# Performance work log

Measured on AMD Instinct MI355X. Metric: run time of the kernel, lower is better.

## Reference

```python
import jax, jax.numpy as jnp
import numpy as np

N, S, E, H = 4, 2048, 1024, 16
D = E // H  # head dim = 64


def setup_inputs() -> dict:
    key = jax.random.key(0)
    ks = jax.random.split(key, 8)
    return {
        "values": jax.random.normal(ks[0], (N, S, E), dtype=jnp.float32),
        "keys": jax.random.normal(ks[1], (N, S, E), dtype=jnp.float32),
        "queries": jax.random.normal(ks[2], (N, S, E), dtype=jnp.float32),
        "mask": jnp.ones((N, 1, 1, S), dtype=jnp.int32),
        "Wv": jax.random.normal(ks[3], (D, D), dtype=jnp.float32) / np.sqrt(D),
        "Wk": jax.random.normal(ks[4], (D, D), dtype=jnp.float32) / np.sqrt(D),
        "Wq": jax.random.normal(ks[5], (D, D), dtype=jnp.float32) / np.sqrt(D),
        "W_out": jax.random.normal(ks[6], (E, E), dtype=jnp.float32) / np.sqrt(E),
        "b_out": jnp.zeros((E,), dtype=jnp.float32),
    }


def reference(values, keys, queries, mask, Wv, Wk, Wq, W_out, b_out):
    n, q_len = queries.shape[0], queries.shape[1]
    v = values.reshape(n, -1, H, D)
    k = keys.reshape(n, -1, H, D)
    q = queries.reshape(n, q_len, H, D)
    # per-head linear projections (torch Linear: x @ W.T), shared across heads
    v = jnp.einsum('nlhd,ed->nlhe', v, Wv)
    k = jnp.einsum('nlhd,ed->nlhe', k, Wk)
    q = jnp.einsum('nqhd,ed->nqhe', q, Wq)
    # full score tensor [n, h, q, k], faithful to the original einsum
    energy = jnp.einsum('nqhd,nkhd->nhqk', q, k)
    energy = jnp.where(mask == 0, jnp.float32(-1e20), energy)
    # NOTE: original scales by sqrt(embed_size), not sqrt(head_dim)
    attention = jax.nn.softmax(energy / jnp.sqrt(jnp.float32(E)), axis=3)
    out = jnp.einsum('nhql,nlhd->nqhd', attention, v).reshape(n, q_len, E)
    out = out @ W_out.T + b_out
    return out
```

## Files before the change

### kernel.cpp

```cpp
#include <hip/hip_runtime.h>
#include <stdint.h>

#define N_B 4
#define SEQ 2048
#define EMB 1024
#define NH  16
#define HD  64
#define NHT 64
#define BQ  128
#define BK  64

typedef __attribute__((ext_vector_type(8))) short bf16x8;
typedef __attribute__((ext_vector_type(4))) short bf16x4;
typedef __attribute__((ext_vector_type(4))) float f32x4;

__device__ __forceinline__ short f2bf(float x) {
  unsigned u = __float_as_uint(x);
  u += 0x7fffu + ((u >> 16) & 1u);
  return (short)(u >> 16);
}

#if __has_builtin(__builtin_amdgcn_cvt_pk_bf16_f32)
typedef __attribute__((ext_vector_type(2))) __bf16 bf16v2;
__device__ __forceinline__ unsigned pkbf(float a, float b) {
  bf16v2 r = __builtin_amdgcn_cvt_pk_bf16_f32(a, b);
  union { bf16v2 v; unsigned u; } c; c.v = r; return c.u;
}
#else
__device__ __forceinline__ unsigned pkbf(float a, float b) {
  return (unsigned)(unsigned short)f2bf(a) | ((unsigned)(unsigned short)f2bf(b) << 16);
}
#endif

__device__ __forceinline__ void glds16(const short* g, short* l) {
  __builtin_amdgcn_global_load_lds(
      (const __attribute__((address_space(1))) unsigned int*)g,
      (__attribute__((address_space(3))) unsigned int*)l, 16, 0, 0);
}

__device__ __forceinline__ int swz_src(int lane) {
  return (((lane & 7) ^ ((lane >> 3) & 7)) * 8) + ((lane >> 3) * 64);
}
__device__ __forceinline__ int swz_rd(int r, int k) {
  return r * 64 + ((k ^ (r & 7)) * 8);
}

__global__ __launch_bounds__(256) void projm_kernel(
    const float* __restrict__ Xq, const float* __restrict__ Xk, const float* __restrict__ Xv,
    const float* __restrict__ Wq, const float* __restrict__ Wk, const float* __restrict__ Wv,
    short* __restrict__ Qp, short* __restrict__ Kp, short* __restrict__ Vp,
    const float* __restrict__ Wo, short* __restrict__ Wb) {
  int tid = threadIdx.x;
  int z = blockIdx.z;
  if (z == 3) {
    int flat = blockIdx.x + blockIdx.y * 16;
    int idx = (flat * 256 + tid) * 4;
    f32x4 v = *(const f32x4*)(Wo + idx);
    uint2 u; u.x = pkbf(v.x, v.y); u.y = pkbf(v.z, v.w);
    *(uint2*)(Wb + idx) = u;
    return;
  }
  const float* X = (z == 0) ? Xq : (z == 1) ? Xk : Xv;
  const float* W = (z == 0) ? Wq : (z == 1) ? Wk : Wv;
  short* out = (z == 0) ? Qp : (z == 1) ? Kp : Vp;
  int transposed = (z == 2);

  __shared__ __attribute__((aligned(16))) short Xs[128 * 64];
  __shared__ __attribute__((aligned(16))) short Ws[64 * 64];
  int w = tid >> 6, lane = tid & 63;
  int quad = lane >> 4, l15 = lane & 15;
  int sb = blockIdx.x * 128;
  int nh = blockIdx.y;
  int n = nh >> 4, h = nh & 15;
  int r4 = tid >> 2, c0 = (tid & 3) * 16;
  int ch0 = c0 >> 3;
#pragma unroll
  for (int rr = 0; rr < 2; rr++) {
    int row = rr * 64 + r4;
    const float* gp = X + ((size_t)(n * SEQ + sb + row)) * EMB + h * HD + c0;
    f32x4 a = *(const f32x4*)gp, b = *(const f32x4*)(gp + 4);
    f32x4 c = *(const f32x4*)(gp + 8), d = *(const f32x4*)(gp + 12);
    uint4 u0, u1;
    u0.x = pkbf(a.x, a.y); u0.y = pkbf(a.z, a.w);
    u0.z = pkbf(b.x, b.y); u0.w = pkbf(b.z, b.w);
    u1.x = pkbf(c.x, c.y); u1.y = pkbf(c.z, c.w);
    u1.z = pkbf(d.x, d.y); u1.w = pkbf(d.z, d.w);
    *(uint4*)&Xs[row * 64 + ((ch0 ^ (row & 7)) * 8)] = u0;
    *(uint4*)&Xs[row * 64 + (((ch0 + 1) ^ (row & 7)) * 8)] = u1;
  }
  {
    int e = r4;
    const float* wp = W + e * HD + c0;
    f32x4 a = *(const f32x4*)wp, b = *(const f32x4*)(wp + 4);
    f32x4 c = *(const f32x4*)(wp + 8), d = *(const f32x4*)(wp + 12);
    uint4 u0, u1;
    u0.x = pkbf(a.x, a.y); u0.y = pkbf(a.z, a.w);
    u0.z = pkbf(b.x, b.y); u0.w = pkbf(b.z, b.w);
    u1.x = pkbf(c.x, c.y); u1.y = pkbf(c.z, c.w);
    u1.z = pkbf(d.x, d.y); u1.w = pkbf(d.z, d.w);
    *(uint4*)&Ws[e * 64 + ((ch0 ^ (e & 7)) * 8)] = u0;
    *(uint4*)&Ws[e * 64 + (((ch0 + 1) ^ (e & 7)) * 8)] = u1;
  }
  __syncthreads();
  f32x4 acc[2][4] = {};
#pragma unroll
  for (int ch = 0; ch < 2; ch++) {
    bf16x8 af[2], bfr[4];
#pragma unroll
    for (int mi = 0; mi < 2; mi++)
      af[mi] = *(const bf16x8*)&Xs[swz_rd(w * 32 + mi * 16 + l15, ch * 4 + quad)];
#pragma unroll
    for (int ni = 0; ni < 4; ni++)
      bfr[ni] = *(const bf16x8*)&Ws[swz_rd(ni * 16 + l15, ch * 4 + quad)];
#pragma unroll
    for (int mi = 0; mi < 2; mi++)
#pragma unroll
      for (int ni = 0; ni < 4; ni++)
        acc[mi][ni] = __builtin_amdgcn_mfma_f32_16x16x32_bf16(af[mi], bfr[ni], acc[mi][ni], 0, 0, 0);
  }
  if (!transposed) {
#pragma unroll
    for (int mi = 0; mi < 2; mi++)
#pragma unroll
      for (int ni = 0; ni < 4; ni++)
#pragma unroll
        for (int r = 0; r < 4; r++) {
          int s = sb + w * 32 + mi * 16 + quad * 4 + r;
          out[((size_t)nh * SEQ + s) * HD + ni * 16 + l15] = f2bf(acc[mi][ni][r]);
        }
  } else {
#pragma unroll
    for (int mi = 0; mi < 2; mi++)
#pragma unroll
      for (int ni = 0; ni < 4; ni++) {
        int e2 = ni * 16 + l15;
        int s0 = sb + w * 32 + mi * 16 + quad * 4;
        uint2 u;
        u.x = pkbf(acc[mi][ni][0], acc[mi][ni][1]);
        u.y = pkbf(acc[mi][ni][2], acc[mi][ni][3]);
        *(uint2*)(out + ((size_t)nh * HD + e2) * SEQ + s0) = u;
      }
  }
}

__global__ __launch_bounds__(256, 4) void attn_kernel(
    const short* __restrict__ Qg, const short* __restrict__ Kg,
    const short* __restrict__ Vg, const int* __restrict__ maskp,
    short* __restrict__ AO) {
  __shared__ __attribute__((aligned(16))) short Ks[64 * 64];
  __shared__ __attribute__((aligned(16))) short Vts[64 * 64];
  __shared__ __attribute__((aligned(16))) short QP[128 * 64];

  int tid = threadIdx.x;
  int w = tid >> 6, lane = tid & 63;
  int quad = lane >> 4, l15 = lane & 15;
  int nh = blockIdx.x;
  int qt0 = blockIdx.y * BQ;
  int n = nh >> 4, h = nh & 15;
  const float csc = 0.04508422f;
  int ssrc = swz_src(lane);
  int vrow = lane >> 3;
  int vcg = (((lane & 7) ^ ((lane >> 3) & 7)) * 8);
  const int NT = SEQ / BK;

  const short* kb = Kg + (size_t)nh * SEQ * HD;
  const short* vb = Vg + (size_t)nh * HD * SEQ;

  const short* qbase = Qg + ((size_t)nh * SEQ + qt0) * HD;
#pragma unroll
  for (int i = 0; i < 4; i++) {
    int idx = (w * 4 + i) * 512;
    glds16(qbase + idx + ssrc, &QP[idx]);
  }
  int mcur = maskp[n * SEQ + lane];
  __syncthreads();
  bf16x8 qf[2][2];
#pragma unroll
  for (int nt = 0; nt < 2; nt++)
#pragma unroll
    for (int ch = 0; ch < 2; ch++)
      qf[nt][ch] = *(const bf16x8*)&QP[swz_rd(w * 32 + nt * 16 + l15, ch * 4 + quad)];

  bf16x8 vone;
#pragma unroll
  for (int j = 0; j < 8; j++) vone[j] = (short)0x3F80;

  f32x4 Oacc[2][4] = {};
  f32x4 lacc[2] = {};
  short* psw = &QP[w * 2048];

  for (int kt = 0; kt < NT; kt++) {
    int k0 = kt * BK;
    __syncthreads();
#pragma unroll
    for (int i = 0; i < 2; i++) {
      int idx = (w * 2 + i) * 512;
      glds16(kb + (size_t)k0 * HD + idx + ssrc, &Ks[idx]);
      int d = (w * 2 + i) * 8 + vrow;
      glds16(vb + (size_t)d * SEQ + k0 + vcg, &Vts[idx]);
    }
    int knx = (kt + 1 < NT) ? kt + 1 : kt;
    int mnxt = maskp[n * SEQ + knx * BK + lane];
    __syncthreads();

    unsigned long long mb = __ballot(mcur != 0);

    f32x4 st[4][2];
#pragma unroll
    for (int mt = 0; mt < 4; mt++) {
      bf16x8 kf0 = *(const bf16x8*)&Ks[swz_rd(mt * 16 + l15, quad)];
      bf16x8 kf1 = *(const bf16x8*)&Ks[swz_rd(mt * 16 + l15, 4 + quad)];
#pragma unroll
      for (int nt = 0; nt < 2; nt++) {
        f32x4 a = {0.f, 0.f, 0.f, 0.f};
        a = __builtin_amdgcn_mfma_f32_16x16x32_bf16(kf0, qf[nt][0], a, 0, 0, 0);
        a = __builtin_amdgcn_mfma_f32_16x16x32_bf16(kf1, qf[nt][1], a, 0, 0, 0);
        st[mt][nt] = a;
      }
    }
    if (mb != ~0ull) {
#pragma unroll
      for (int mt = 0; mt < 4; mt++)
#pragma unroll
        for (int r = 0; r < 4; r++) {
          int kk = mt * 16 + quad * 4 + r;
          if (!((mb >> kk) & 1)) { st[mt][0][r] = -1e20f; st[mt][1][r] = -1e20f; }
        }
    }
#pragma unroll
    for (int nt = 0; nt < 2; nt++) {
      int wrow = nt * 16 + l15;
#pragma unroll
      for (int mt = 0; mt < 4; mt++) {
        float p0 = __builtin_amdgcn_exp2f(st[mt][nt][0] * csc);
        float p1 = __builtin_amdgcn_exp2f(st[mt][nt][1] * csc);
        float p2 = __builtin_amdgcn_exp2f(st[mt][nt][2] * csc);
        float p3 = __builtin_amdgcn_exp2f(st[mt][nt][3] * csc);
        uint2 u;
        u.x = pkbf(p0, p1);
        u.y = pkbf(p2, p3);
        *(uint2*)&psw[wrow * 64 + (((mt * 2 + (quad >> 1)) ^ (wrow & 7)) * 8) + (quad & 1) * 4] = u;
      }
    }
    __builtin_amdgcn_wave_barrier();

#pragma unroll
    for (int ch = 0; ch < 2; ch++) {
      bf16x8 pf[2];
#pragma unroll
      for (int qt = 0; qt < 2; qt++)
        pf[qt] = *(const bf16x8*)&psw[swz_rd(qt * 16 + l15, ch * 4 + quad)];
#pragma unroll
      for (int qt = 0; qt < 2; qt++)
        lacc[qt] = __builtin_amdgcn_mfma_f32_16x16x32_bf16(pf[qt], vone, lacc[qt], 0, 0, 0);
#pragma unroll
      for (int dt = 0; dt < 4; dt++) {
        bf16x8 vf = *(const bf16x8*)&Vts[swz_rd(dt * 16 + l15, ch * 4 + quad)];
#pragma unroll
        for (int qt = 0; qt < 2; qt++)
          Oacc[qt][dt] = __builtin_amdgcn_mfma_f32_16x16x32_bf16(pf[qt], vf, Oacc[qt][dt], 0, 0, 0);
      }
    }
    mcur = mnxt;
  }
#pragma unroll
  for (int qt = 0; qt < 2; qt++)
#pragma unroll
    for (int r = 0; r < 4; r++) {
      float inv = 1.0f / lacc[qt][r];
      int qrow = qt0 + w * 32 + qt * 16 + quad * 4 + r;
      size_t rowb = ((size_t)n * SEQ + qrow) * EMB + h * HD;
#pragma unroll
      for (int dt = 0; dt < 4; dt++)
        AO[rowb + dt * 16 + l15] = f2bf(Oacc[qt][dt][r] * inv);
    }
}

__global__ __launch_bounds__(256, 2) void gemm_kernel(const short* __restrict__ A,
                                                      const short* __restrict__ B,
                                                      const float* __restrict__ bias,
                                                      float* __restrict__ C) {
  __shared__ __attribute__((aligned(16))) short As[2][128 * 64];
  __shared__ __attribute__((aligned(16))) short Bs[2][128 * 64];
  int tid = threadIdx.x;
  int w = tid >> 6, lane = tid & 63;
  int quad = lane >> 4, l15 = lane & 15;
  int m0 = blockIdx.x * 128, n0 = blockIdx.y * 128;
  int mw = (w & 1) * 64, nw = (w >> 1) * 64;
  int lrow = lane >> 3;
  int lcg = ((lane & 7) ^ ((lane >> 3) & 7)) * 8;
  f32x4 acc[4][4] = {};
#pragma unroll
  for (int i = 0; i < 4; i++) {
    int ii = w * 4 + i;
    int r = ii * 8 + lrow;
    glds16(A + (size_t)(m0 + r) * 1024 + lcg, &As[0][ii * 512]);
    glds16(B + (size_t)(n0 + r) * 1024 + lcg, &Bs[0][ii * 512]);
  }
  __syncthreads();
  for (int kt = 0; kt < 16; kt++) {
    int cur = kt & 1;
    if (kt < 15) {
      int k0n = (kt + 1) * 64;
#pragma unroll
      for (int i = 0; i < 4; i++) {
        int ii = w * 4 + i;
        int r = ii * 8 + lrow;
        glds16(A + (size_t)(m0 + r) * 1024 + k0n + lcg, &As[cur ^ 1][ii * 512]);
        glds16(B + (size_t)(n0 + r) * 1024 + k0n + lcg, &Bs[cur ^ 1][ii * 512]);
      }
    }
#pragma unroll
    for (int ch = 0; ch < 2; ch++) {
      bf16x8 af[4], bfr[4];
#pragma unroll
      for (int mi = 0; mi < 4; mi++)
        af[mi] = *(const bf16x8*)&As[cur][swz_rd(mw + mi * 16 + l15, ch * 4 + quad)];
#pragma unroll
      for (int ni = 0; ni < 4; ni++)
        bfr[ni] = *(const bf16x8*)&Bs[cur][swz_rd(nw + ni * 16 + l15, ch * 4 + quad)];
#pragma unroll
      for (int mi = 0; mi < 4; mi++)
#pragma unroll
        for (int ni = 0; ni < 4; ni++)
          acc[mi][ni] = __builtin_amdgcn_mfma_f32_16x16x32_bf16(af[mi], bfr[ni], acc[mi][ni], 0, 0, 0);
    }
    __syncthreads();
  }
#pragma unroll
  for (int ni = 0; ni < 4; ni++) {
    int col = n0 + nw + ni * 16 + l15;
    float bv = bias[col];
#pragma unroll
    for (int mi = 0; mi < 4; mi++) {
      int rb = m0 + mw + mi * 16 + quad * 4;
#pragma unroll
      for (int r = 0; r < 4; r++)
        C[(size_t)(rb + r) * 1024 + col] = acc[mi][ni][r] + bv;
    }
  }
}

extern "C" void kernel_launch(void* const* d_in, const int* in_sizes, int n_in,
                              void* d_out, int out_size, void* d_ws, size_t ws_size,
                              hipStream_t stream) {
  const float* values  = (const float*)d_in[0];
  const float* keys    = (const float*)d_in[1];
  const float* queries = (const float*)d_in[2];
  const int*   mask    = (const int*)d_in[3];
  const float* Wv = (const float*)d_in[4];
  const float* Wk = (const float*)d_in[5];
  const float* Wq = (const float*)d_in[6];
  const float* Wo = (const float*)d_in[7];
  const float* bo = (const float*)d_in[8];
  float* out = (float*)d_out;

  short* ws = (short*)d_ws;
  short* Qp = ws;
  short* Kp = Qp + (size_t)NHT * SEQ * HD;
  short* Vp = Kp + (size_t)NHT * SEQ * HD;
  short* AO = Vp + (size_t)NHT * SEQ * HD;
  short* Wb = AO + (size_t)N_B * SEQ * EMB;

  dim3 pg(SEQ / 128, NHT, 4);
  projm_kernel<<<pg, dim3(256), 0, stream>>>(queries, keys, values, Wq, Wk, Wv,
                                             Qp, Kp, Vp, Wo, Wb);
  dim3 ag(NHT, SEQ / BQ);
  attn_kernel<<<ag, dim3(256), 0, stream>>>(Qp, Kp, Vp, mask, AO);
  dim3 gg(8192 / 128, 1024 / 128);
  gemm_kernel<<<gg, dim3(256), 0, stream>>>(AO, Wb, bo, out);
}
```

Baseline: 284.0 us.

## Double-buffer K/V tiles in attention and fold softmax scale into Q

The attention loop now keeps two K/V tile buffers in one shared LDS array. It prefetches the next tile while computing on the current one, so each iteration needs one block barrier instead of two. The P staging buffer is split into two halves per wave, and s_setprio is raised around the MFMA sections. The softmax scale is applied in the Q projection before bf16 rounding, which removes one multiply per score. The cost is more LDS per block, and Q is rounded after scaling, which shifts precision slightly.

```diff
diff --git a/kernel.cpp b/kernel.cpp
--- a/kernel.cpp
+++ b/kernel.cpp
@@ -64,6 +64,7 @@
   const float* W = (z == 0) ? Wq : (z == 1) ? Wk : Wv;
   short* out = (z == 0) ? Qp : (z == 1) ? Kp : Vp;
   int transposed = (z == 2);
+  float oscale = (z == 0) ? 0.04508422f : 1.0f;
 
   __shared__ __attribute__((aligned(16))) short Xs[128 * 64];
   __shared__ __attribute__((aligned(16))) short Ws[64 * 64];
@@ -126,7 +127,7 @@
 #pragma unroll
         for (int r = 0; r < 4; r++) {
           int s = sb + w * 32 + mi * 16 + quad * 4 + r;
-          out[((size_t)nh * SEQ + s) * HD + ni * 16 + l15] = f2bf(acc[mi][ni][r]);
+          out[((size_t)nh * SEQ + s) * HD + ni * 16 + l15] = f2bf(acc[mi][ni][r] * oscale);
         }
   } else {
 #pragma unroll
@@ -147,9 +148,7 @@
     const short* __restrict__ Qg, const short* __restrict__ Kg,
     const short* __restrict__ Vg, const int* __restrict__ maskp,
     short* __restrict__ AO) {
-  __shared__ __attribute__((aligned(16))) short Ks[64 * 64];
-  __shared__ __attribute__((aligned(16))) short Vts[64 * 64];
-  __shared__ __attribute__((aligned(16))) short QP[128 * 64];
+  __shared__ __attribute__((aligned(16))) short L[20480];
 
   int tid = threadIdx.x;
   int w = tid >> 6, lane = tid & 63;
@@ -157,7 +156,6 @@
   int nh = blockIdx.x;
   int qt0 = blockIdx.y * BQ;
   int n = nh >> 4, h = nh & 15;
-  const float csc = 0.04508422f;
   int ssrc = swz_src(lane);
   int vrow = lane >> 3;
   int vcg = (((lane & 7) ^ ((lane >> 3) & 7)) * 8);
@@ -165,12 +163,20 @@
 
   const short* kb = Kg + (size_t)nh * SEQ * HD;
   const short* vb = Vg + (size_t)nh * HD * SEQ;
+  short* Pw = &L[16384 + w * 1024];
 
   const short* qbase = Qg + ((size_t)nh * SEQ + qt0) * HD;
 #pragma unroll
   for (int i = 0; i < 4; i++) {
     int idx = (w * 4 + i) * 512;
-    glds16(qbase + idx + ssrc, &QP[idx]);
+    glds16(qbase + idx + ssrc, &L[8192 + idx]);
+  }
+#pragma unroll
+  for (int i = 0; i < 2; i++) {
+    int idx = (w * 2 + i) * 512;
+    glds16(kb + idx + ssrc, &L[idx]);
+    int d = (w * 2 + i) * 8 + vrow;
+    glds16(vb + (size_t)d * SEQ + vcg, &L[4096 + idx]);
   }
   int mcur = maskp[n * SEQ + lane];
   __syncthreads();
@@ -179,7 +185,8 @@
   for (int nt = 0; nt < 2; nt++)
 #pragma unroll
     for (int ch = 0; ch < 2; ch++)
-      qf[nt][ch] = *(const bf16x8*)&QP[swz_rd(w * 32 + nt * 16 + l15, ch * 4 + quad)];
+      qf[nt][ch] = *(const bf16x8*)&L[8192 + swz_rd(w * 32 + nt * 16 + l15, ch * 4 + quad)];
+  __syncthreads();
 
   bf16x8 vone;
 #pragma unroll
@@ -187,81 +194,95 @@
 
   f32x4 Oacc[2][4] = {};
   f32x4 lacc[2] = {};
-  short* psw = &QP[w * 2048];
 
   for (int kt = 0; kt < NT; kt++) {
-    int k0 = kt * BK;
-    __syncthreads();
-#pragma unroll
-    for (int i = 0; i < 2; i++) {
-      int idx = (w * 2 + i) * 512;
-      glds16(kb + (size_t)k0 * HD + idx + ssrc, &Ks[idx]);
-      int d = (w * 2 + i) * 8 + vrow;
-      glds16(vb + (size_t)d * SEQ + k0 + vcg, &Vts[idx]);
+    int cur = kt & 1;
+    const short* Kb = &L[cur * 8192];
+    const short* Vb = &L[cur * 8192 + 4096];
+    if (kt + 1 < NT) {
+      size_t k0n = (size_t)(kt + 1) * BK;
+      short* Kn = &L[(cur ^ 1) * 8192];
+#pragma unroll
+      for (int i = 0; i < 2; i++) {
+        int idx = (w * 2 + i) * 512;
+        glds16(kb + k0n * HD + idx + ssrc, &Kn[idx]);
+        int d = (w * 2 + i) * 8 + vrow;
+        glds16(vb + (size_t)d * SEQ + k0n + vcg, &Kn[4096 + idx]);
+      }
     }
     int knx = (kt + 1 < NT) ? kt + 1 : kt;
     int mnxt = maskp[n * SEQ + knx * BK + lane];
-    __syncthreads();
 
     unsigned long long mb = __ballot(mcur != 0);
-
-    f32x4 st[4][2];
-#pragma unroll
-    for (int mt = 0; mt < 4; mt++) {
-      bf16x8 kf0 = *(const bf16x8*)&Ks[swz_rd(mt * 16 + l15, quad)];
-      bf16x8 kf1 = *(const bf16x8*)&Ks[swz_rd(mt * 16 + l15, 4 + quad)];
+    bool anymask = (mb != ~0ull);
+
+#pragma unroll
+    for (int half = 0; half < 2; half++) {
+      f32x4 st[2][2];
+      __builtin_amdgcn_s_setprio(1);
+#pragma unroll
+      for (int m2 = 0; m2 < 2; m2++) {
+        int mt = half * 2 + m2;
+        bf16x8 kf0 = *(const bf16x8*)&Kb[swz_rd(mt * 16 + l15, quad)];
+        bf16x8 kf1 = *(const bf16x8*)&Kb[swz_rd(mt * 16 + l15, 4 + quad)];
+#pragma unroll
+        for (int nt = 0; nt < 2; nt++) {
+          f32x4 a = {0.f, 0.f, 0.f, 0.f};
+          a = __builtin_amdgcn_mfma_f32_16x16x32_bf16(kf0, qf[nt][0], a, 0, 0, 0);
+          a = __builtin_amdgcn_mfma_f32_16x16x32_bf16(kf1, qf[nt][1], a, 0, 0, 0);
+          st[m2][nt] = a;
+        }
+      }
+      __builtin_amdgcn_s_setprio(0);
+      if (anymask) {
+#pragma unroll
+        for (int m2 = 0; m2 < 2; m2++)
+#pragma unroll
+          for (int r = 0; r < 4; r++) {
+            int kk = (half * 2 + m2) * 16 + quad * 4 + r;
+            if (!((mb >> kk) & 1)) { st[m2][0][r] = -1e20f; st[m2][1][r] = -1e20f; }
+          }
+      }
 #pragma unroll
       for (int nt = 0; nt < 2; nt++) {
-        f32x4 a = {0.f, 0.f, 0.f, 0.f};
-        a = __builtin_amdgcn_mfma_f32_16x16x32_bf16(kf0, qf[nt][0], a, 0, 0, 0);
-        a = __builtin_amdgcn_mfma_f32_16x16x32_bf16(kf1, qf[nt][1], a, 0, 0, 0);
-        st[mt][nt] = a;
-      }
-    }
-    if (mb != ~0ull) {
-#pragma unroll
-      for (int mt = 0; mt < 4; mt++)
-#pragma unroll
-        for (int r = 0; r < 4; r++) {
-          int kk = mt * 16 + quad * 4 + r;
-          if (!((mb >> kk) & 1)) { st[mt][0][r] = -1e20f; st[mt][1][r] = -1e20f; }
+        int row = nt * 16 + l15;
+#pragma unroll
+        for (int m2 = 0; m2 < 2; m2++) {
+          float p0 = __builtin_amdgcn_exp2f(st[m2][nt][0]);
+          float p1 = __builtin_amdgcn_exp2f(st[m2][nt][1]);
+          float p2 = __builtin_amdgcn_exp2f(st[m2][nt][2]);
+          float p3 = __builtin_amdgcn_exp2f(st[m2][nt][3]);
+          uint2 u;
+          u.x = pkbf(p0, p1);
+          u.y = pkbf(p2, p3);
+          int chunk = m2 * 2 + (quad >> 1);
+          *(uint2*)&Pw[row * 32 + ((chunk ^ (row & 3)) * 8) + (quad & 1) * 4] = u;
         }
-    }
-#pragma unroll
-    for (int nt = 0; nt < 2; nt++) {
-      int wrow = nt * 16 + l15;
-#pragma unroll
-      for (int mt = 0; mt < 4; mt++) {
-        float p0 = __builtin_amdgcn_exp2f(st[mt][nt][0] * csc);
-        float p1 = __builtin_amdgcn_exp2f(st[mt][nt][1] * csc);
-        float p2 = __builtin_amdgcn_exp2f(st[mt][nt][2] * csc);
-        float p3 = __builtin_amdgcn_exp2f(st[mt][nt][3] * csc);
-        uint2 u;
-        u.x = pkbf(p0, p1);
-        u.y = pkbf(p2, p3);
-        *(uint2*)&psw[wrow * 64 + (((mt * 2 + (quad >> 1)) ^ (wrow & 7)) * 8) + (quad & 1) * 4] = u;
-      }
-    }
-    __builtin_amdgcn_wave_barrier();
-
-#pragma unroll
-    for (int ch = 0; ch < 2; ch++) {
+      }
+      __builtin_amdgcn_wave_barrier();
+
+      __builtin_amdgcn_s_setprio(1);
       bf16x8 pf[2];
 #pragma unroll
-      for (int qt = 0; qt < 2; qt++)
-        pf[qt] = *(const bf16x8*)&psw[swz_rd(qt * 16 + l15, ch * 4 + quad)];
+      for (int qt = 0; qt < 2; qt++) {
+        int row = qt * 16 + l15;
+        pf[qt] = *(const bf16x8*)&Pw[row * 32 + ((quad ^ (row & 3)) * 8)];
+      }
 #pragma unroll
       for (int qt = 0; qt < 2; qt++)
         lacc[qt] = __builtin_amdgcn_mfma_f32_16x16x32_bf16(pf[qt], vone, lacc[qt], 0, 0, 0);
 #pragma unroll
       for (int dt = 0; dt < 4; dt++) {
-        bf16x8 vf = *(const bf16x8*)&Vts[swz_rd(dt * 16 + l15, ch * 4 + quad)];
+        bf16x8 vf = *(const bf16x8*)&Vb[swz_rd(dt * 16 + l15, half * 4 + quad)];
 #pragma unroll
         for (int qt = 0; qt < 2; qt++)
           Oacc[qt][dt] = __builtin_amdgcn_mfma_f32_16x16x32_bf16(pf[qt], vf, Oacc[qt][dt], 0, 0, 0);
       }
+      __builtin_amdgcn_s_setprio(0);
+      __builtin_amdgcn_wave_barrier();
     }
     mcur = mnxt;
+    __syncthreads();
   }
 #pragma unroll
   for (int qt = 0; qt < 2; qt++)
```

New measurement: 274.6 us. -3.3%, faster.
